# Optimization experiments

Hardware: AMD Instinct MI355X
Metric: run time of the kernel (lower is better)

The kernel has to match this reference:

```python
import jax, jax.numpy as jnp
import numpy as np

N_CLASS, N_SUPPORT, N_QUERY = 64, 5, 64
D_IN, C, WIN = 1024, 128, 5
D = C * WIN * WIN  # 3200, fine-encoder output dim


def setup_inputs() -> dict:
    key = jax.random.key(0)
    ks = jax.random.split(key, 6)
    s = 0.02  # weight init scale
    return {
        "xs": jax.random.normal(ks[0], (N_CLASS, N_SUPPORT, D_IN), jnp.float32),
        "xq": jax.random.normal(ks[1], (N_CLASS, N_QUERY, D_IN), jnp.float32),
        "W_share": jax.random.normal(ks[2], (D_IN, D), jnp.float32) * s,
        "b_share": jnp.zeros((D,), jnp.float32),
        "W_att": jax.random.normal(ks[3], (C, C), jnp.float32) * s,
        "b_att": jnp.zeros((C,), jnp.float32),
        "W_fine": jax.random.normal(ks[4], (D, D), jnp.float32) * s,
        "b_fine": jnp.zeros((D,), jnp.float32),
    }


def reference(xs, xq, W_share, b_share, W_att, b_att, W_fine, b_fine):
    n_class, n_support = xs.shape[0], xs.shape[1]
    n_query = xq.shape[1]
    ns = n_class * n_support

    # concat support + query, run shared encoder
    x = jnp.concatenate([xs.reshape(ns, -1), xq.reshape(n_class * n_query, -1)], axis=0)
    z_share = jax.nn.relu(x @ W_share + b_share)            # [N, D]
    z4 = z_share.reshape(-1, C, WIN, WIN)

    # attention head: spatial mean -> linear -> per-channel logits
    z_att = z4.mean(axis=(2, 3)) @ W_att + b_att            # [N, C]

    diag_c = jax.nn.softmax(z_att[:ns].mean(axis=0)) * C    # [C]
    w = jnp.repeat(diag_c, WIN * WIN)                       # [D] diagonal of learned metric

    # fine encoder (flatten + linear)
    z = z_share @ W_fine + b_fine                           # [N, D]
    z_proto = z[:ns].reshape(n_class, n_support, -1).mean(axis=1)  # [n_class, D]
    zq = z[ns:]                                             # [n, D]

    # attentionMetric with diagonal metric == weighted squared distance:
    # dists[i,j] = sum_d w_d (zq_i - proto_j)^2, expanded to avoid the n*m*d diff tensor
    q2 = (zq * zq) @ w                                      # [n]
    p2 = (z_proto * z_proto) @ w                            # [m]
    cross = (zq * w) @ z_proto.T                            # [n, m]
    dists = q2[:, None] + p2[None, :] - 2.0 * cross         # [n, m]

    log_p_y = jax.nn.log_softmax(-dists, axis=1).reshape(n_class, n_query, n_class)
    target = jnp.arange(n_class)
    tgt = jnp.broadcast_to(target[:, None, None], (n_class, n_query, 1))
    loss_val = -jnp.take_along_axis(log_p_y, tgt, axis=2).mean()
    y_hat = jnp.argmax(log_p_y, axis=2)
    acc_val = (y_hat == target[:, None]).astype(jnp.float32).mean()
    return loss_val, acc_val
```

## Files before the change

### kernel.cpp

```cpp
#include <hip/hip_runtime.h>
#include <math.h>

#define N_CLASS 64
#define N_SUPPORT 5
#define N_QUERY 64
#define D_IN 1024
#define C_CH 128
#define WIN 5
#define D_FEAT 3200
#define NS 320
#define NQ 4096
#define M_ROWS 4416
#define M_PAD 4480

#define ZP_SLICE  (N_CLASS * D_FEAT)
#define GT_SLICE  (128 * D_FEAT)
#define CR_SLICE  (NQ * 128)
#define NKS       10
#define LOSS_BLKS (NQ / 4)

#define PREP_X   4480
#define PREP_WS  3200
#define CONV_WF  10000

#define WS_SCALE    64.0f
#define WS_INVSCALE 0.015625f

#define WS_XF8      0u
#define WS_WSF8     4718592u
#define WS_ZSB      8126464u
#define WS_WFB      36388864u
#define WS_WFTB     56868864u
#define WS_ARENA    77348864u
#define WS_UB       98320384u
#define WS_YB       99139584u
#define WS_GT       99958784u
#define WS_WV       100777984u
#define WS_P2       100790784u
#define WS_CVEC     100791296u
#define WS_LPART    100791808u

typedef __bf16 bf16x8 __attribute__((ext_vector_type(8)));
typedef __bf16 bf16x4 __attribute__((ext_vector_type(4)));
typedef float floatx4 __attribute__((ext_vector_type(4)));
typedef __attribute__((address_space(1))) const void* gptr_t;
typedef __attribute__((address_space(3))) void* lptr_t;

__device__ __forceinline__ float waveReduceSum(float v) {
    for (int off = 32; off > 0; off >>= 1) v += __shfl_xor(v, off, 64);
    return v;
}

__global__ __launch_bounds__(256) void prep_kernel(const float* __restrict__ xs,
                                                   const float* __restrict__ xq,
                                                   const float* __restrict__ W_share,
                                                   unsigned char* __restrict__ Xf8,
                                                   unsigned char* __restrict__ Wsf8)
{
    __shared__ float tile[32][33];
    const int b = blockIdx.x;
    const int t = threadIdx.x;

    if (b < PREP_X) {
        const int e = (b * 256 + t) * 4;
        const int row = e >> 10;
        const int col = e & 1023;
        float4 v = make_float4(0.f, 0.f, 0.f, 0.f);
        if (row < NS)          v = *(const float4*)(xs + (size_t)row * D_IN + col);
        else if (row < M_ROWS) v = *(const float4*)(xq + (size_t)(row - NS) * D_IN + col);
        int p = __builtin_amdgcn_cvt_pk_fp8_f32(v.x, v.y, 0, false);
        p     = __builtin_amdgcn_cvt_pk_fp8_f32(v.z, v.w, p, true);
        const int ocol = col ^ (((row >> 1) & 1) << 3);
        *(int*)(Xf8 + (size_t)row * D_IN + ocol) = p;
        return;
    }
    const int tx = t & 31;
    const int ty = t >> 5;
    const int tb = b - PREP_X;
    const int n0 = (tb % 100) * 32;
    const int k0 = (tb / 100) * 32;
#pragma unroll
    for (int i = ty; i < 32; i += 8)
        tile[i][tx] = W_share[(size_t)(k0 + i) * D_FEAT + n0 + tx];
    __syncthreads();
#pragma unroll
    for (int i = ty; i < 32; i += 8) {
        const int p = __builtin_amdgcn_cvt_pk_fp8_f32(tile[tx][i] * WS_SCALE, 0.f,
                                                      0, false);
        const int n = n0 + i;
        const int k = (k0 + tx) ^ (((n >> 1) & 1) << 3);
        Wsf8[(size_t)n * D_IN + k] = (unsigned char)(p & 0xff);
    }
}

__global__ __launch_bounds__(256, 3) void gemm_fp8_128(const unsigned char* __restrict__ A,
                                                       const unsigned char* __restrict__ Bt,
                                                       const float* __restrict__ bias,
                                                       __bf16* __restrict__ out_bf)
{
    __shared__ __align__(16) unsigned char smem[49152];

    const int t    = threadIdx.x;
    const int lane = t & 63;
    const int w    = t >> 6;
    const int wm   = w >> 1;
    const int wn   = w & 1;

    const int bx = blockIdx.x % 25;
    const int by = blockIdx.x / 25;
    const int bm = by * 128;
    const int bn = bx * 128;

    const int q    = lane >> 4;
    const int r16  = lane & 15;
    const int m3   = (r16 >> 1) & 7;
    const int off0 = (q ^ m3) * 8;

    const int rowA = (wm * 64 + r16) * 64;
    const int rowB = (wn * 64 + r16) * 64;

    const int srow  = t >> 2;
    const int sunit = 16 * ((t & 3) ^ ((srow >> 2) & 3));

    const unsigned char* gA = A  + (size_t)(bm + srow) * D_IN + sunit;
    const unsigned char* gB = Bt + (size_t)(bn + srow) * D_IN + sunit;

    auto stage = [&](int uu, int slot) {
        const unsigned char* ga = gA + uu * 64;
        const unsigned char* gb = gB + uu * 64;
        unsigned char* l = smem + slot * 16384 + t * 16;
        __builtin_amdgcn_global_load_lds((gptr_t)ga,           (lptr_t)l,            16, 0, 0);
        __builtin_amdgcn_global_load_lds((gptr_t)(ga + 65536), (lptr_t)(l + 4096),   16, 0, 0);
        __builtin_amdgcn_global_load_lds((gptr_t)gb,           (lptr_t)(l + 8192),   16, 0, 0);
        __builtin_amdgcn_global_load_lds((gptr_t)(gb + 65536), (lptr_t)(l + 12288),  16, 0, 0);
    };

    floatx4 acc[4][4] = {};
    long av[4], bv[4];

    auto ld_frags = [&](const unsigned char* sa, int o) {
#pragma unroll
        for (int mi = 0; mi < 4; ++mi)
            av[mi] = *(const long*)(sa + rowA + mi * 1024 + o);
#pragma unroll
        for (int ni = 0; ni < 4; ++ni)
            bv[ni] = *(const long*)(sa + 8192 + rowB + ni * 1024 + o);
    };
    auto mfma16 = [&]() {
#pragma unroll
        for (int mi = 0; mi < 4; ++mi)
#pragma unroll
            for (int ni = 0; ni < 4; ++ni)
                acc[mi][ni] = __builtin_amdgcn_mfma_f32_16x16x32_fp8_fp8(
                    av[mi], bv[ni], acc[mi][ni], 0, 0, 0);
    };

    stage(0, 0);
    stage(1, 1);
    asm volatile("s_waitcnt vmcnt(4)" ::: "memory");
    __builtin_amdgcn_s_barrier();

    int sl = 0;
    for (int u = 0; u < 14; ++u) {
        const unsigned char* sa = smem + sl * 16384;
        ld_frags(sa, off0);
        stage(u + 2, sl == 0 ? 2 : sl - 1);
        __builtin_amdgcn_s_barrier();
        asm volatile("s_waitcnt lgkmcnt(0)" ::: "memory");
        __builtin_amdgcn_s_setprio(1);
        mfma16();
        __builtin_amdgcn_s_setprio(0);
        __builtin_amdgcn_s_barrier();
        ld_frags(sa, off0 ^ 32);
        asm volatile("s_waitcnt vmcnt(4)" ::: "memory");
        __builtin_amdgcn_s_barrier();
        asm volatile("s_waitcnt lgkmcnt(0)" ::: "memory");
        __builtin_amdgcn_s_setprio(1);
        mfma16();
        __builtin_amdgcn_s_setprio(0);
        __builtin_amdgcn_s_barrier();
        sl = sl == 2 ? 0 : sl + 1;
    }
    {
        const unsigned char* sa = smem + sl * 16384;
        ld_frags(sa, off0);       mfma16();
        ld_frags(sa, off0 ^ 32);  mfma16();
        sl = sl == 2 ? 0 : sl + 1;
    }
    asm volatile("s_waitcnt vmcnt(0)" ::: "memory");
    __builtin_amdgcn_s_barrier();
    {
        const unsigned char* sa = smem + sl * 16384;
        ld_frags(sa, off0);       mfma16();
        ld_frags(sa, off0 ^ 32);  mfma16();
    }

    __syncthreads();
    float bcol[4];
#pragma unroll
    for (int ni = 0; ni < 4; ++ni) bcol[ni] = bias[bn + wn * 64 + ni * 16 + r16];
    const int ebase = (wm * 64 + q * 4) * 256 + wn * 128 + r16 * 2;
#pragma unroll
    for (int mi = 0; mi < 4; ++mi)
#pragma unroll
        for (int ni = 0; ni < 4; ++ni) {
            const int cb = (ni ^ q) << 5;
#pragma unroll
            for (int reg = 0; reg < 4; ++reg) {
                float v = acc[mi][ni][reg] * WS_INVSCALE + bcol[ni];
                v = fmaxf(v, 0.f);
                *(__bf16*)(smem + ebase + mi * 4096 + reg * 256 + cb) = (__bf16)v;
            }
        }
    __syncthreads();
#pragma unroll
    for (int ps = 0; ps < 8; ++ps) {
        const int idx  = ps * 256 + t;
        const int row  = idx >> 4;
        const int grow = bm + row;
        if (grow < M_ROWS) {
            const int lb = row * 256 + (((idx & 15) << 4) ^ (((row >> 2) & 3) << 5));
            const int4 d = *(const int4*)(smem + lb);
            *(int4*)((char*)out_bf + ((size_t)grow * D_FEAT + bn + (idx & 15) * 8) * 2) = d;
        }
    }
}

__global__ __launch_bounds__(256) void gemm_bf16(const __bf16* __restrict__ A,
                                                 const __bf16* __restrict__ Bt,
                                                 const float* __restrict__ bias,
                                                 __bf16* __restrict__ out_bf,
                                                 float* __restrict__ out_f32,
                                                 int N, int strideK, int kIters,
                                                 int Mout, int relu, int sliceStride,
                                                 int nbx, int nby)
{
    __shared__ __align__(16) char smem[32768];

    int bx, by, ks;
    {
        const int nbxy = nbx * nby;
        ks = blockIdx.x / nbxy;
        const int b = blockIdx.x - ks * nbxy;
        const int fg = nbx >> 3;
        const int full = fg * 8 * nby;
        if (b < full) {
            const int g = b / (8 * nby);
            const int r = b - g * 8 * nby;
            bx = g * 8 + (r & 7);
            by = r >> 3;
        } else {
            const int rem = nbx - fg * 8;
            const int r = b - full;
            bx = fg * 8 + r % rem;
            by = r / rem;
        }
    }

    const int t    = threadIdx.x;
    const int lane = t & 63;
    const int w    = t >> 6;
    const int wm   = w >> 1;
    const int wn   = w & 1;
    const int bm   = by * 128;
    const int bn   = bx * 128;

    const int q    = lane >> 4;
    const int r16  = lane & 15;
    const int sw   = (r16 >> 1) & 3;
    const int cA   = (q ^ sw) * 8;

    const int srow   = w * 16 + (lane >> 2);
    const int sglob8 = (((lane & 3) ^ ((lane >> 3) & 3))) * 8;

    const int kBase = ks * kIters * 64;
    floatx4 acc[4][4] = {};

    for (int ki = 0; ki < kIters; ++ki) {
        const int k0 = kBase + ki * 64;
        __syncthreads();
#pragma unroll
        for (int s = 0; s < 2; ++s) {
#pragma unroll
            for (int j = 0; j < 2; ++j) {
                const __bf16* ga = A  + (size_t)(bm + j * 64 + srow) * strideK
                                      + k0 + s * 32 + sglob8;
                const __bf16* gb = Bt + (size_t)(bn + j * 64 + srow) * strideK
                                      + k0 + s * 32 + sglob8;
                char* la = smem +         s * 8192 + (j * 256 + w * 64) * 16;
                char* lb = smem + 16384 + s * 8192 + (j * 256 + w * 64) * 16;
                __builtin_amdgcn_global_load_lds((gptr_t)ga, (lptr_t)la, 16, 0, 0);
                __builtin_amdgcn_global_load_lds((gptr_t)gb, (lptr_t)lb, 16, 0, 0);
            }
        }
        __syncthreads();

#pragma unroll
        for (int s = 0; s < 2; ++s) {
            const __bf16* sAe = (const __bf16*)(smem +         s * 8192);
            const __bf16* sBe = (const __bf16*)(smem + 16384 + s * 8192);
            bf16x8 av[4], bv[4];
#pragma unroll
            for (int mi = 0; mi < 4; ++mi)
                av[mi] = *(const bf16x8*)(sAe + ((wm * 64 + mi * 16 + r16) * 32 + cA));
#pragma unroll
            for (int ni = 0; ni < 4; ++ni)
                bv[ni] = *(const bf16x8*)(sBe + ((wn * 64 + ni * 16 + r16) * 32 + cA));
#pragma unroll
            for (int mi = 0; mi < 4; ++mi)
#pragma unroll
                for (int ni = 0; ni < 4; ++ni)
                    acc[mi][ni] = __builtin_amdgcn_mfma_f32_16x16x32_bf16(
                        av[mi], bv[ni], acc[mi][ni], 0, 0, 0);
        }
    }

#pragma unroll
    for (int ni = 0; ni < 4; ++ni) {
        const int col = bn + wn * 64 + ni * 16 + r16;
        const float bcol = sliceStride ? 0.f : bias[col];
#pragma unroll
        for (int mi = 0; mi < 4; ++mi) {
#pragma unroll
            for (int reg = 0; reg < 4; ++reg) {
                const int row = bm + wm * 64 + mi * 16 + q * 4 + reg;
                if (row < Mout) {
                    if (sliceStride) {
                        out_f32[(size_t)ks * sliceStride + (size_t)row * N + col] =
                            acc[mi][ni][reg];
                    } else {
                        float v = acc[mi][ni][reg] + bcol;
                        if (relu) v = fmaxf(v, 0.f);
                        if (out_f32) out_f32[(size_t)row * N + col] = v;
                        else         out_bf [(size_t)row * N + col] = (__bf16)v;
                    }
                }
            }
        }
    }
}

__global__ __launch_bounds__(256) void ut_conv_kernel(const __bf16* __restrict__ z_share,
                                                      const float* __restrict__ W_fine,
                                                      __bf16* __restrict__ u,
                                                      float* __restrict__ upool,
                                                      __bf16* __restrict__ Wfb,
                                                      __bf16* __restrict__ WfTb)
{
    __shared__ __align__(16) char smem_u[D_FEAT * 4];
    const int b = blockIdx.x;
    const int t = threadIdx.x;

    if (b >= 128) {
        float (*tile)[33] = (float(*)[33])smem_u;
        const int tb = b - 128;
        const int tx = t & 31;
        const int ty = t >> 5;
        const int n0 = (tb % 100) * 32;
        const int k0 = (tb / 100) * 32;
#pragma unroll
        for (int i = ty; i < 32; i += 8) {
            const float v = W_fine[(size_t)(k0 + i) * D_FEAT + n0 + tx];
            Wfb[(size_t)(k0 + i) * D_FEAT + n0 + tx] = (__bf16)v;
            tile[i][tx] = v;
        }
        __syncthreads();
#pragma unroll
        for (int i = ty; i < 32; i += 8)
            WfTb[(size_t)(n0 + i) * D_FEAT + k0 + tx] = (__bf16)tile[tx][i];
        return;
    }

    float* srow_ = (float*)smem_u;
    const int p = b;
    if (p >= N_CLASS) {
        for (int k = t; k < D_FEAT; k += 256) u[(size_t)p * D_FEAT + k] = (__bf16)0.f;
        return;
    }
    const __bf16* base = z_share + (size_t)(p * N_SUPPORT) * D_FEAT;
    for (int k = t; k < D_FEAT; k += 256) {
        float s = 0.f;
#pragma unroll
        for (int ss = 0; ss < N_SUPPORT; ++ss) s += (float)base[(size_t)ss * D_FEAT + k];
        s *= (1.0f / N_SUPPORT);
        u[(size_t)p * D_FEAT + k] = (__bf16)s;
        srow_[k] = s;
    }
    __syncthreads();
    if (t < C_CH) {
        float pool = 0.f;
#pragma unroll
        for (int win = 0; win < 25; ++win) pool += srow_[t * 25 + win];
        upool[(size_t)p * C_CH + t] = pool;
    }
}

__global__ __launch_bounds__(128) void att2_kernel(const float* __restrict__ upool,
                                                   const float* __restrict__ W_att,
                                                   const float* __restrict__ b_att,
                                                   float* __restrict__ wvec)
{
    __shared__ float s_pm[C_CH];
    __shared__ float s_att[C_CH];
    __shared__ float s_diag[C_CH];
    const int c = threadIdx.x;
    float a = 0.f;
    for (int p = 0; p < N_CLASS; ++p) a += upool[(size_t)p * C_CH + c];
    s_pm[c] = a * (1.0f / (N_CLASS * 25));
    __syncthreads();
    float acc = b_att[c];
    for (int k = 0; k < C_CH; ++k) acc += s_pm[k] * W_att[k * C_CH + c];
    s_att[c] = acc;
    __syncthreads();
    float m = -INFINITY;
    for (int k = 0; k < C_CH; ++k) m = fmaxf(m, s_att[k]);
    float s = 0.f;
    for (int k = 0; k < C_CH; ++k) s += expf(s_att[k] - m);
    s_diag[c] = expf(acc - m) / s * (float)C_CH;
    __syncthreads();
    for (int j = c; j < D_FEAT; j += C_CH) wvec[j] = s_diag[j / 25];
}

__global__ __launch_bounds__(256) void y_kernel(const float* __restrict__ zp_part,
                                                const float* __restrict__ wv,
                                                const float* __restrict__ bf,
                                                __bf16* __restrict__ y,
                                                float* __restrict__ p2,
                                                float* __restrict__ cvec)
{
    __shared__ float s_red2[8];
    const int p = blockIdx.x;
    const int t = threadIdx.x;
    if (p >= N_CLASS) {
        for (int j = t; j < D_FEAT; j += 256) y[(size_t)p * D_FEAT + j] = (__bf16)0.f;
        return;
    }
    float s2 = 0.f, sc = 0.f;
    for (int j = t; j < D_FEAT; j += 256) {
        float zpf = bf[j];
#pragma unroll
        for (int ss = 0; ss < NKS; ++ss)
            zpf += zp_part[(size_t)ss * ZP_SLICE + (size_t)p * D_FEAT + j];
        const float wj = wv[j];
        y[(size_t)p * D_FEAT + j] = (__bf16)(wj * zpf);
        s2 += wj * zpf * zpf;
        sc += bf[j] * wj * zpf;
    }
    s2 = waveReduceSum(s2);
    sc = waveReduceSum(sc);
    const int lane = t & 63, wid = t >> 6;
    if (lane == 0) { s_red2[wid] = s2; s_red2[4 + wid] = sc; }
    __syncthreads();
    if (t == 0) {
        p2[p]   = s_red2[0] + s_red2[1] + s_red2[2] + s_red2[3];
        cvec[p] = s_red2[4] + s_red2[5] + s_red2[6] + s_red2[7];
    }
}

__global__ __launch_bounds__(256) void gtsum_kernel(const float* __restrict__ gp,
                                                    __bf16* __restrict__ Gt)
{
    const int i4 = blockIdx.x * 256 + threadIdx.x;
    if (i4 >= GT_SLICE / 4) return;
    float4 s = make_float4(0.f, 0.f, 0.f, 0.f);
#pragma unroll
    for (int ss = 0; ss < NKS; ++ss) {
        const float4 v = *(const float4*)(gp + (size_t)ss * GT_SLICE + i4 * 4);
        s.x += v.x; s.y += v.y; s.z += v.z; s.w += v.w;
    }
    bf16x4 o = { (__bf16)s.x, (__bf16)s.y, (__bf16)s.z, (__bf16)s.w };
    *(bf16x4*)(Gt + (size_t)i4 * 4) = o;
}

__global__ __launch_bounds__(256) void loss_kernel(const float* __restrict__ cross_part,
                                                   const float* __restrict__ p2,
                                                   const float* __restrict__ cvec,
                                                   float* __restrict__ lpart)
{
    __shared__ float s_l[4], s_a[4];
    const int t = threadIdx.x;
    const int lane = t & 63, wid = t >> 6;
    const int i = blockIdx.x * 4 + wid;
    float cr = 0.f;
#pragma unroll
    for (int ss = 0; ss < NKS; ++ss)
        cr += cross_part[(size_t)ss * CR_SLICE + (size_t)i * 128 + lane];
    const float neg = 2.0f * (cr + cvec[lane]) - p2[lane];
    float m = neg;
    for (int off = 32; off > 0; off >>= 1) m = fmaxf(m, __shfl_xor(m, off, 64));
    float e = expf(neg - m);
    float ssum = e;
    for (int off = 32; off > 0; off >>= 1) ssum += __shfl_xor(ssum, off, 64);
    const float lse = m + logf(ssum);
    const int tcls = i >> 6;
    const float negt = __shfl(neg, tcls, 64);
    float v = -neg; int bi = lane;
    for (int off = 32; off > 0; off >>= 1) {
        const float ov = __shfl_xor(v, off, 64);
        const int   oi = __shfl_xor(bi, off, 64);
        if (ov < v || (ov == v && oi < bi)) { v = ov; bi = oi; }
    }
    if (lane == 0) { s_l[wid] = lse - negt; s_a[wid] = (bi == tcls) ? 1.0f : 0.0f; }
    __syncthreads();
    if (t == 0) {
        lpart[blockIdx.x]             = s_l[0] + s_l[1] + s_l[2] + s_l[3];
        lpart[LOSS_BLKS + blockIdx.x] = s_a[0] + s_a[1] + s_a[2] + s_a[3];
    }
}

__global__ __launch_bounds__(256) void writeout_kernel(const float* __restrict__ lpart,
                                                       float* __restrict__ out)
{
    __shared__ float s_red2[8];
    const int t = threadIdx.x;
    float l = 0.f, a = 0.f;
    for (int k = t; k < LOSS_BLKS; k += 256) {
        l += lpart[k];
        a += lpart[LOSS_BLKS + k];
    }
    l = waveReduceSum(l);
    a = waveReduceSum(a);
    const int lane = t & 63, wid = t >> 6;
    if (lane == 0) { s_red2[wid] = l; s_red2[4 + wid] = a; }
    __syncthreads();
    if (t == 0) {
        out[0] = (s_red2[0] + s_red2[1] + s_red2[2] + s_red2[3]) * (1.0f / NQ);
        out[1] = (s_red2[4] + s_red2[5] + s_red2[6] + s_red2[7]) * (1.0f / NQ);
    }
}

extern "C" void kernel_launch(void* const* d_in, const int* in_sizes, int n_in,
                              void* d_out, int out_size, void* d_ws, size_t ws_size,
                              hipStream_t stream)
{
    const float* xs      = (const float*)d_in[0];
    const float* xq      = (const float*)d_in[1];
    const float* W_share = (const float*)d_in[2];
    const float* b_share = (const float*)d_in[3];
    const float* W_att   = (const float*)d_in[4];
    const float* b_att   = (const float*)d_in[5];
    const float* W_fine  = (const float*)d_in[6];
    const float* b_fine  = (const float*)d_in[7];
    float* out = (float*)d_out;

    char* ws = (char*)d_ws;
    unsigned char* Xf8  = (unsigned char*)(ws + WS_XF8);
    unsigned char* Wsf8 = (unsigned char*)(ws + WS_WSF8);
    __bf16* Zsb     = (__bf16*)(ws + WS_ZSB);
    __bf16* Wfb     = (__bf16*)(ws + WS_WFB);
    __bf16* WfTb    = (__bf16*)(ws + WS_WFTB);
    float*  arena   = (float*) (ws + WS_ARENA);
    float*  upool   = arena;
    float*  zp_part = arena;
    float*  gt_part = arena;
    float*  cr_part = arena;
    __bf16* ub      = (__bf16*)(ws + WS_UB);
    __bf16* yb      = (__bf16*)(ws + WS_YB);
    __bf16* Gt      = (__bf16*)(ws + WS_GT);
    float*  wv      = (float*) (ws + WS_WV);
    float*  p2v     = (float*) (ws + WS_P2);
    float*  cvec    = (float*) (ws + WS_CVEC);
    float*  lpart   = (float*) (ws + WS_LPART);

    prep_kernel<<<PREP_X + PREP_WS, 256, 0, stream>>>(xs, xq, W_share, Xf8, Wsf8);

    gemm_fp8_128<<<35 * 25, 256, 0, stream>>>(Xf8, Wsf8, b_share, Zsb);

    ut_conv_kernel<<<128 + CONV_WF, 256, 0, stream>>>(Zsb, W_fine, ub, upool,
                                                      Wfb, WfTb);
    att2_kernel<<<1, C_CH, 0, stream>>>(upool, W_att, b_att, wv);

    gemm_bf16<<<25 * NKS, 256, 0, stream>>>(
        ub, WfTb, nullptr, nullptr, zp_part,
        D_FEAT, D_FEAT, 5, N_CLASS, 0, ZP_SLICE, 25, 1);

    y_kernel<<<128, 256, 0, stream>>>(zp_part, wv, b_fine, yb, p2v, cvec);

    gemm_bf16<<<25 * NKS, 256, 0, stream>>>(
        yb, Wfb, nullptr, nullptr, gt_part,
        D_FEAT, D_FEAT, 5, 128, 0, GT_SLICE, 25, 1);

    gtsum_kernel<<<(GT_SLICE / 4 + 255) / 256, 256, 0, stream>>>(gt_part, Gt);

    gemm_bf16<<<32 * NKS, 256, 0, stream>>>(
        Zsb + (size_t)NS * D_FEAT, Gt, nullptr, nullptr, cr_part,
        128, D_FEAT, 5, NQ, 0, CR_SLICE, 1, 32);

    loss_kernel<<<LOSS_BLKS, 256, 0, stream>>>(cr_part, p2v, cvec, lpart);

    writeout_kernel<<<1, 256, 0, stream>>>(lpart, out);
}
```

Measured before the change: 238.0 us.

## Fold small kernels into GEMMs via last-block reductions and restructure FP8 GEMM loop

Removes the att2, gtsum and writeout launches. The attention softmax now runs in an extra block of the first bf16 GEMM. The split-K slice sum for Gt and the final loss reduction are done by the last-arriving block, found with atomic counters that prep_kernel clears. The FP8 GEMM main loop also loads both k-halves of fragments at once and issues 32 MFMAs per stage with one barrier instead of three. This cuts launch and sync overhead at the cost of more registers and atomic/fence traffic.

Result: slower. 280.3 us (+17.8%).

```diff
diff --git a/kernel.cpp b/kernel.cpp
--- a/kernel.cpp
+++ b/kernel.cpp
@@ -39,6 +39,8 @@
 #define WS_P2       100790784u
 #define WS_CVEC     100791296u
 #define WS_LPART    100791808u
+#define WS_CNT      100800000u
+#define WS_UPOOL    100800128u
 
 typedef __bf16 bf16x8 __attribute__((ext_vector_type(8)));
 typedef __bf16 bf16x4 __attribute__((ext_vector_type(4)));
@@ -55,13 +57,15 @@
                                                    const float* __restrict__ xq,
                                                    const float* __restrict__ W_share,
                                                    unsigned char* __restrict__ Xf8,
-                                                   unsigned char* __restrict__ Wsf8)
+                                                   unsigned char* __restrict__ Wsf8,
+                                                   int* __restrict__ cnts)
 {
     __shared__ float tile[32][33];
     const int b = blockIdx.x;
     const int t = threadIdx.x;
 
     if (b < PREP_X) {
+        if (b == 0 && t < 32) cnts[t] = 0;
         const int e = (b * 256 + t) * 4;
         const int row = e >> 10;
         const int col = e & 1023;
@@ -136,63 +140,66 @@
     };
 
     floatx4 acc[4][4] = {};
-    long av[4], bv[4];
-
-    auto ld_frags = [&](const unsigned char* sa, int o) {
+    long av0[4], bv0[4], av1[4], bv1[4];
+
+    auto ld16 = [&](const unsigned char* sa) {
 #pragma unroll
         for (int mi = 0; mi < 4; ++mi)
-            av[mi] = *(const long*)(sa + rowA + mi * 1024 + o);
+            av0[mi] = *(const long*)(sa + rowA + mi * 1024 + off0);
 #pragma unroll
         for (int ni = 0; ni < 4; ++ni)
-            bv[ni] = *(const long*)(sa + 8192 + rowB + ni * 1024 + o);
+            bv0[ni] = *(const long*)(sa + 8192 + rowB + ni * 1024 + off0);
+#pragma unroll
+        for (int mi = 0; mi < 4; ++mi)
+            av1[mi] = *(const long*)(sa + rowA + mi * 1024 + (off0 ^ 32));
+#pragma unroll
+        for (int ni = 0; ni < 4; ++ni)
+            bv1[ni] = *(const long*)(sa + 8192 + rowB + ni * 1024 + (off0 ^ 32));
     };
-    auto mfma16 = [&]() {
+    auto mfma32 = [&]() {
+        __builtin_amdgcn_s_setprio(1);
 #pragma unroll
         for (int mi = 0; mi < 4; ++mi)
 #pragma unroll
             for (int ni = 0; ni < 4; ++ni)
                 acc[mi][ni] = __builtin_amdgcn_mfma_f32_16x16x32_fp8_fp8(
-                    av[mi], bv[ni], acc[mi][ni], 0, 0, 0);
+                    av0[mi], bv0[ni], acc[mi][ni], 0, 0, 0);
+#pragma unroll
+        for (int mi = 0; mi < 4; ++mi)
+#pragma unroll
+            for (int ni = 0; ni < 4; ++ni)
+                acc[mi][ni] = __builtin_amdgcn_mfma_f32_16x16x32_fp8_fp8(
+                    av1[mi], bv1[ni], acc[mi][ni], 0, 0, 0);
+        __builtin_amdgcn_s_setprio(0);
     };
 
     stage(0, 0);
     stage(1, 1);
-    asm volatile("s_waitcnt vmcnt(4)" ::: "memory");
-    __builtin_amdgcn_s_barrier();
-
-    int sl = 0;
+
     for (int u = 0; u < 14; ++u) {
-        const unsigned char* sa = smem + sl * 16384;
-        ld_frags(sa, off0);
-        stage(u + 2, sl == 0 ? 2 : sl - 1);
-        __builtin_amdgcn_s_barrier();
-        asm volatile("s_waitcnt lgkmcnt(0)" ::: "memory");
-        __builtin_amdgcn_s_setprio(1);
-        mfma16();
-        __builtin_amdgcn_s_setprio(0);
-        __builtin_amdgcn_s_barrier();
-        ld_frags(sa, off0 ^ 32);
+        const unsigned char* sa = smem + (u % 3) * 16384;
         asm volatile("s_waitcnt vmcnt(4)" ::: "memory");
         __builtin_amdgcn_s_barrier();
+        ld16(sa);
+        stage(u + 2, (u + 2) % 3);
         asm volatile("s_waitcnt lgkmcnt(0)" ::: "memory");
-        __builtin_amdgcn_s_setprio(1);
-        mfma16();
-        __builtin_amdgcn_s_setprio(0);
+        mfma32();
+    }
+    {
+        const unsigned char* sa = smem + (14 % 3) * 16384;
+        asm volatile("s_waitcnt vmcnt(4)" ::: "memory");
         __builtin_amdgcn_s_barrier();
-        sl = sl == 2 ? 0 : sl + 1;
+        ld16(sa);
+        asm volatile("s_waitcnt lgkmcnt(0)" ::: "memory");
+        mfma32();
     }
     {
-        const unsigned char* sa = smem + sl * 16384;
-        ld_frags(sa, off0);       mfma16();
-        ld_frags(sa, off0 ^ 32);  mfma16();
-        sl = sl == 2 ? 0 : sl + 1;
-    }
-    asm volatile("s_waitcnt vmcnt(0)" ::: "memory");
-    __builtin_amdgcn_s_barrier();
-    {
-        const unsigned char* sa = smem + sl * 16384;
-        ld_frags(sa, off0);       mfma16();
-        ld_frags(sa, off0 ^ 32);  mfma16();
+        const unsigned char* sa = smem + (15 % 3) * 16384;
+        asm volatile("s_waitcnt vmcnt(0)" ::: "memory");
+        __builtin_amdgcn_s_barrier();
+        ld16(sa);
+        asm volatile("s_waitcnt lgkmcnt(0)" ::: "memory");
+        mfma32();
     }
 
     __syncthreads();
@@ -233,9 +240,58 @@
                                                  float* __restrict__ out_f32,
                                                  int N, int strideK, int kIters,
                                                  int Mout, int relu, int sliceStride,
-                                                 int nbx, int nby)
+                                                 int nbx, int nby,
+                                                 const float* __restrict__ attUpool,
+                                                 const float* __restrict__ W_att,
+                                                 const float* __restrict__ b_att,
+                                                 float* __restrict__ wvec,
+                                                 __bf16* __restrict__ gsumDst,
+                                                 int* __restrict__ cnts)
 {
     __shared__ __align__(16) char smem[32768];
+    __shared__ int s_last;
+
+    const int t = threadIdx.x;
+
+    if (attUpool != nullptr && blockIdx.x == gridDim.x - 1) {
+        float* sW   = (float*)smem;
+        float* s_pm = (float*)(smem + 16384);
+        float* s_at = (float*)(smem + 16384 + 512);
+        float* s_dg = (float*)(smem + 16384 + 1024);
+        if (t < C_CH) {
+            float a = 0.f;
+            for (int p = 0; p < N_CLASS; ++p) a += attUpool[(size_t)p * C_CH + t];
+            s_pm[t] = a * (1.0f / (N_CLASS * 25));
+        }
+        __syncthreads();
+        float acc = (t < C_CH) ? b_att[t] : 0.f;
+#pragma unroll
+        for (int qtr = 0; qtr < 4; ++qtr) {
+            const float4* src = (const float4*)(W_att + qtr * 32 * C_CH);
+            float4* dst = (float4*)sW;
+#pragma unroll
+            for (int i = 0; i < 4; ++i) dst[i * 256 + t] = src[i * 256 + t];
+            __syncthreads();
+            if (t < C_CH) {
+#pragma unroll
+                for (int k = 0; k < 32; ++k)
+                    acc += s_pm[qtr * 32 + k] * sW[k * C_CH + t];
+            }
+            __syncthreads();
+        }
+        if (t < C_CH) s_at[t] = acc;
+        __syncthreads();
+        if (t < C_CH) {
+            float m = -INFINITY;
+            for (int k = 0; k < C_CH; ++k) m = fmaxf(m, s_at[k]);
+            float s = 0.f;
+            for (int k = 0; k < C_CH; ++k) s += expf(s_at[k] - m);
+            s_dg[t] = expf(acc - m) / s * (float)C_CH;
+        }
+        __syncthreads();
+        for (int j = t; j < D_FEAT; j += 256) wvec[j] = s_dg[j / 25];
+        return;
+    }
 
     int bx, by, ks;
     {
@@ -257,7 +313,6 @@
         }
     }
 
-    const int t    = threadIdx.x;
     const int lane = t & 63;
     const int w    = t >> 6;
     const int wm   = w >> 1;
@@ -338,6 +393,31 @@
             }
         }
     }
+
+    if (gsumDst != nullptr) {
+        __syncthreads();
+        __threadfence();
+        if (t == 0) s_last = (atomicAdd(&cnts[by * nbx + bx], 1) == NKS - 1);
+        __syncthreads();
+        if (s_last) {
+            __threadfence();
+#pragma unroll
+            for (int it = 0; it < 16; ++it) {
+                const int e4  = it * 256 + t;
+                const int row = e4 >> 5;
+                const int c4  = (e4 & 31) * 4;
+                float4 s = make_float4(0.f, 0.f, 0.f, 0.f);
+#pragma unroll
+                for (int ss2 = 0; ss2 < NKS; ++ss2) {
+                    const float4 v = *(const float4*)(out_f32 + (size_t)ss2 * sliceStride
+                                        + (size_t)row * N + bn + c4);
+                    s.x += v.x; s.y += v.y; s.z += v.z; s.w += v.w;
+                }
+                bf16x4 o = { (__bf16)s.x, (__bf16)s.y, (__bf16)s.z, (__bf16)s.w };
+                *(bf16x4*)(gsumDst + (size_t)row * N + bn + c4) = o;
+            }
+        }
+    }
 }
 
 __global__ __launch_bounds__(256) void ut_conv_kernel(const __bf16* __restrict__ z_share,
@@ -393,32 +473,6 @@
         for (int win = 0; win < 25; ++win) pool += srow_[t * 25 + win];
         upool[(size_t)p * C_CH + t] = pool;
     }
-}
-
-__global__ __launch_bounds__(128) void att2_kernel(const float* __restrict__ upool,
-                                                   const float* __restrict__ W_att,
-                                                   const float* __restrict__ b_att,
-                                                   float* __restrict__ wvec)
-{
-    __shared__ float s_pm[C_CH];
-    __shared__ float s_att[C_CH];
-    __shared__ float s_diag[C_CH];
-    const int c = threadIdx.x;
-    float a = 0.f;
-    for (int p = 0; p < N_CLASS; ++p) a += upool[(size_t)p * C_CH + c];
-    s_pm[c] = a * (1.0f / (N_CLASS * 25));
-    __syncthreads();
-    float acc = b_att[c];
-    for (int k = 0; k < C_CH; ++k) acc += s_pm[k] * W_att[k * C_CH + c];
-    s_att[c] = acc;
-    __syncthreads();
-    float m = -INFINITY;
-    for (int k = 0; k < C_CH; ++k) m = fmaxf(m, s_att[k]);
-    float s = 0.f;
-    for (int k = 0; k < C_CH; ++k) s += expf(s_att[k] - m);
-    s_diag[c] = expf(acc - m) / s * (float)C_CH;
-    __syncthreads();
-    for (int j = c; j < D_FEAT; j += C_CH) wvec[j] = s_diag[j / 25];
 }
 
 __global__ __launch_bounds__(256) void y_kernel(const float* __restrict__ zp_part,
@@ -457,27 +511,15 @@
     }
 }
 
-__global__ __launch_bounds__(256) void gtsum_kernel(const float* __restrict__ gp,
-                                                    __bf16* __restrict__ Gt)
-{
-    const int i4 = blockIdx.x * 256 + threadIdx.x;
-    if (i4 >= GT_SLICE / 4) return;
-    float4 s = make_float4(0.f, 0.f, 0.f, 0.f);
-#pragma unroll
-    for (int ss = 0; ss < NKS; ++ss) {
-        const float4 v = *(const float4*)(gp + (size_t)ss * GT_SLICE + i4 * 4);
-        s.x += v.x; s.y += v.y; s.z += v.z; s.w += v.w;
-    }
-    bf16x4 o = { (__bf16)s.x, (__bf16)s.y, (__bf16)s.z, (__bf16)s.w };
-    *(bf16x4*)(Gt + (size_t)i4 * 4) = o;
-}
-
 __global__ __launch_bounds__(256) void loss_kernel(const float* __restrict__ cross_part,
                                                    const float* __restrict__ p2,
                                                    const float* __restrict__ cvec,
-                                                   float* __restrict__ lpart)
+                                                   float* __restrict__ lpart,
+                                                   int* __restrict__ cnt,
+                                                   float* __restrict__ out)
 {
     __shared__ float s_l[4], s_a[4];
+    __shared__ int s_last;
     const int t = threadIdx.x;
     const int lane = t & 63, wid = t >> 6;
     const int i = blockIdx.x * 4 + wid;
@@ -505,14 +547,12 @@
     if (t == 0) {
         lpart[blockIdx.x]             = s_l[0] + s_l[1] + s_l[2] + s_l[3];
         lpart[LOSS_BLKS + blockIdx.x] = s_a[0] + s_a[1] + s_a[2] + s_a[3];
-    }
-}
-
-__global__ __launch_bounds__(256) void writeout_kernel(const float* __restrict__ lpart,
-                                                       float* __restrict__ out)
-{
-    __shared__ float s_red2[8];
-    const int t = threadIdx.x;
+        __threadfence();
+        s_last = (atomicAdd(cnt, 1) == LOSS_BLKS - 1);
+    }
+    __syncthreads();
+    if (!s_last) return;
+    __threadfence();
     float l = 0.f, a = 0.f;
     for (int k = t; k < LOSS_BLKS; k += 256) {
         l += lpart[k];
@@ -520,12 +560,11 @@
     }
     l = waveReduceSum(l);
     a = waveReduceSum(a);
-    const int lane = t & 63, wid = t >> 6;
-    if (lane == 0) { s_red2[wid] = l; s_red2[4 + wid] = a; }
+    if (lane == 0) { s_l[wid] = l; s_a[wid] = a; }
     __syncthreads();
     if (t == 0) {
-        out[0] = (s_red2[0] + s_red2[1] + s_red2[2] + s_red2[3]) * (1.0f / NQ);
-        out[1] = (s_red2[4] + s_red2[5] + s_red2[6] + s_red2[7]) * (1.0f / NQ);
+        out[0] = (s_l[0] + s_l[1] + s_l[2] + s_l[3]) * (1.0f / NQ);
+        out[1] = (s_a[0] + s_a[1] + s_a[2] + s_a[3]) * (1.0f / NQ);
     }
 }
 
@@ -550,7 +589,6 @@
     __bf16* Wfb     = (__bf16*)(ws + WS_WFB);
     __bf16* WfTb    = (__bf16*)(ws + WS_WFTB);
     float*  arena   = (float*) (ws + WS_ARENA);
-    float*  upool   = arena;
     float*  zp_part = arena;
     float*  gt_part = arena;
     float*  cr_part = arena;
@@ -561,32 +599,34 @@
     float*  p2v     = (float*) (ws + WS_P2);
     float*  cvec    = (float*) (ws + WS_CVEC);
     float*  lpart   = (float*) (ws + WS_LPART);
-
-    prep_kernel<<<PREP_X + PREP_WS, 256, 0, stream>>>(xs, xq, W_share, Xf8, Wsf8);
+    int*    cnts    = (int*)   (ws + WS_CNT);
+    float*  upool   = (float*) (ws + WS_UPOOL);
+
+    prep_kernel<<<PREP_X + PREP_WS, 256, 0, stream>>>(xs, xq, W_share, Xf8, Wsf8,
+                                                      cnts);
 
     gemm_fp8_128<<<35 * 25, 256, 0, stream>>>(Xf8, Wsf8, b_share, Zsb);
 
     ut_conv_kernel<<<128 + CONV_WF, 256, 0, stream>>>(Zsb, W_fine, ub, upool,
                                                       Wfb, WfTb);
-    att2_kernel<<<1, C_CH, 0, stream>>>(upool, W_att, b_att, wv);
-
-    gemm_bf16<<<25 * NKS, 256, 0, stream>>>(
+
+    gemm_bf16<<<25 * NKS + 1, 256, 0, stream>>>(
         ub, WfTb, nullptr, nullptr, zp_part,
-        D_FEAT, D_FEAT, 5, N_CLASS, 0, ZP_SLICE, 25, 1);
+        D_FEAT, D_FEAT, 5, N_CLASS, 0, ZP_SLICE, 25, 1,
+        upool, W_att, b_att, wv, nullptr, nullptr);
 
     y_kernel<<<128, 256, 0, stream>>>(zp_part, wv, b_fine, yb, p2v, cvec);
 
     gemm_bf16<<<25 * NKS, 256, 0, stream>>>(
         yb, Wfb, nullptr, nullptr, gt_part,
-        D_FEAT, D_FEAT, 5, 128, 0, GT_SLICE, 25, 1);
-
-    gtsum_kernel<<<(GT_SLICE / 4 + 255) / 256, 256, 0, stream>>>(gt_part, Gt);
+        D_FEAT, D_FEAT, 5, 128, 0, GT_SLICE, 25, 1,
+        nullptr, nullptr, nullptr, nullptr, Gt, cnts);
 
     gemm_bf16<<<32 * NKS, 256, 0, stream>>>(
         Zsb + (size_t)NS * D_FEAT, Gt, nullptr, nullptr, cr_part,
-        128, D_FEAT, 5, NQ, 0, CR_SLICE, 1, 32);
-
-    loss_kernel<<<LOSS_BLKS, 256, 0, stream>>>(cr_part, p2v, cvec, lpart);
-
-    writeout_kernel<<<1, 256, 0, stream>>>(lpart, out);
-}
+        128, D_FEAT, 5, NQ, 0, CR_SLICE, 1, 32,
+        nullptr, nullptr, nullptr, nullptr, nullptr, nullptr);
+
+    loss_kernel<<<LOSS_BLKS, 256, 0, stream>>>(cr_part, p2v, cvec, lpart,
+                                               &cnts[30], out);
+}
```
